# Optimization experiments

Hardware: AMD Instinct MI355X
Metric: run time of the kernel (lower is better)

## Reference

```python
import jax, jax.numpy as jnp
import numpy as np

EPS = 1e-5

def setup_inputs() -> dict:
    key = jax.random.key(0)
    ks = jax.random.split(key, 4)
    B, C, H, W = 32, 256, 32, 32
    x = jax.random.normal(ks[0], (B, C, H, W), dtype=jnp.float32)
    gamma = jnp.ones((C,), dtype=jnp.float32)
    beta = jnp.zeros((C,), dtype=jnp.float32)
    # torch nn.Linear init scale ~ 1/sqrt(fan_in)
    W_kqv = jax.random.normal(ks[1], (3 * C, C), dtype=jnp.float32) / np.sqrt(C)
    b_kqv = jnp.zeros((3 * C,), dtype=jnp.float32)
    W_proj = jax.random.normal(ks[2], (C, C), dtype=jnp.float32) / np.sqrt(C)
    b_proj = jnp.zeros((C,), dtype=jnp.float32)
    return {"x": x, "gamma": gamma, "beta": beta, "W_kqv": W_kqv,
            "b_kqv": b_kqv, "W_proj": W_proj, "b_proj": b_proj}

def reference(x, gamma, beta, W_kqv, b_kqv, W_proj, b_proj):
    B, C, H, W = x.shape
    scale = jnp.sqrt(jnp.asarray(C, dtype=x.dtype))
    # BatchNorm2d (training-mode batch statistics, biased variance, eps=1e-5)
    mean = jnp.mean(x, axis=(0, 2, 3), keepdims=True)
    var = jnp.var(x, axis=(0, 2, 3), keepdims=True)
    t = (x - mean) * jax.lax.rsqrt(var + EPS)
    t = t * gamma[None, :, None, None] + beta[None, :, None, None]
    # [B, C, H, W] -> [B, N, C] with N = H*W
    t = t.reshape(B, C, H * W).transpose(0, 2, 1)
    kqv = t @ W_kqv.T + b_kqv           # [B, N, 3C]
    q, k, v = jnp.split(kqv, 3, axis=-1)  # each [B, N, C]
    s = jnp.einsum('bnc,bmc->bnm', q, k) / scale  # [B, N, N]
    attn = jax.nn.softmax(s, axis=-1)
    o = jnp.einsum('bnm,bmc->bnc', attn, v)        # [B, N, C]
    o = o @ W_proj.T + b_proj
    o = o.transpose(0, 2, 1).reshape(B, C, H, W)
    return o + x
```

## Files before the change

kernel.cpp:

```cpp
#include <hip/hip_runtime.h>

typedef unsigned short u16;
typedef __attribute__((ext_vector_type(8))) short bf16x8;
typedef __attribute__((ext_vector_type(4))) float f32x4;

__device__ __forceinline__ float bf2f(u16 u) {
  union { unsigned u; float f; } c; c.u = ((unsigned)u) << 16; return c.f;
}
__device__ __forceinline__ u16 f2bf(float f) {
  union { float f; unsigned u; } c; c.f = f;
  unsigned u = c.u;
  return (u16)((u + 0x7FFFu + ((u >> 16) & 1u)) >> 16);
}
__device__ __forceinline__ void gld16(const void* g, void* l) {
  __builtin_amdgcn_global_load_lds(
      (__attribute__((address_space(1))) void*)g,
      (__attribute__((address_space(3))) void*)l, 16, 0, 0);
}

#define BB 32
#define CC 256
#define NN 1024

__global__ __launch_bounds__(256) void convert_w_kernel(
    const float* __restrict__ Wk, const float* __restrict__ bk,
    const float* __restrict__ Wp, const float* __restrict__ bp,
    u16* __restrict__ Wkb, u16* __restrict__ bkb,
    u16* __restrict__ Wpb, u16* __restrict__ bpb)
{
  int b = blockIdx.x, t = threadIdx.x;
  const float* src; u16* dst; int idx, n;
  if (b < 768)       { src = Wk; dst = Wkb; idx = b * 256 + t;        n = 196608; }
  else if (b < 771)  { src = bk; dst = bkb; idx = (b - 768) * 256 + t; n = 768;   }
  else if (b < 1027) { src = Wp; dst = Wpb; idx = (b - 771) * 256 + t; n = 65536; }
  else               { src = bp; dst = bpb; idx = t;                  n = 256;    }
  if (idx < n) dst[idx] = f2bf(src[idx]);
}

__global__ __launch_bounds__(256) void bn_stats_kernel(
    const float* __restrict__ x, const float* __restrict__ gamma,
    const float* __restrict__ beta, float* __restrict__ scl, float* __restrict__ sft)
{
  int c = blockIdx.x;
  int tid = threadIdx.x;
  float s = 0.f, q = 0.f;
  for (int g = tid; g < 8192; g += 256) {
    int b = g >> 8;
    int n = (g & 255) * 4;
    float4 v = *reinterpret_cast<const float4*>(x + (((size_t)(b * CC + c)) << 10) + n);
    s += v.x + v.y + v.z + v.w;
    q += v.x * v.x + v.y * v.y + v.z * v.z + v.w * v.w;
  }
  __shared__ float rs[256], rq[256];
  rs[tid] = s; rq[tid] = q;
  __syncthreads();
  for (int off = 128; off > 0; off >>= 1) {
    if (tid < off) { rs[tid] += rs[tid + off]; rq[tid] += rq[tid + off]; }
    __syncthreads();
  }
  if (tid == 0) {
    float mean = rs[0] * (1.f / 32768.f);
    float var  = rq[0] * (1.f / 32768.f) - mean * mean;
    float rstd = rsqrtf(var + 1e-5f);
    float g = gamma[c] * rstd;
    scl[c] = g;
    sft[c] = beta[c] - mean * g;
  }
}

__global__ __launch_bounds__(256) void norm_transpose_kernel(
    const float* __restrict__ x, const float* __restrict__ scl,
    const float* __restrict__ sft, u16* __restrict__ t)
{
  __shared__ float tile[64][65];
  int b = blockIdx.z, n0 = blockIdx.x * 64, c0 = blockIdx.y * 64;
  int tid = threadIdx.x;
  int hi = tid >> 4, lo4 = (tid & 15) * 4;
  #pragma unroll
  for (int r = 0; r < 4; ++r) {
    int cl = r * 16 + hi;
    int c = c0 + cl;
    float4 v = *reinterpret_cast<const float4*>(
        x + (((size_t)(b * CC + c)) << 10) + n0 + lo4);
    float sc = scl[c], sh = sft[c];
    tile[cl][lo4 + 0] = v.x * sc + sh;
    tile[cl][lo4 + 1] = v.y * sc + sh;
    tile[cl][lo4 + 2] = v.z * sc + sh;
    tile[cl][lo4 + 3] = v.w * sc + sh;
  }
  __syncthreads();
  #pragma unroll
  for (int r = 0; r < 4; ++r) {
    int nl = r * 16 + hi;
    ushort4 o;
    o.x = f2bf(tile[lo4 + 0][nl]);
    o.y = f2bf(tile[lo4 + 1][nl]);
    o.z = f2bf(tile[lo4 + 2][nl]);
    o.w = f2bf(tile[lo4 + 3][nl]);
    *reinterpret_cast<ushort4*>(t + ((size_t)(b * NN + n0 + nl)) * CC + c0 + lo4) = o;
  }
}

__global__ __launch_bounds__(256) void gemm_nt_kernel(
    const u16* __restrict__ A, int lda, size_t sA,
    const u16* __restrict__ B, int ldb, size_t sB,
    u16* __restrict__ C, int ldc, size_t sC,
    int K, const u16* __restrict__ bias, float scale, int mode,
    const float* __restrict__ xres, float* __restrict__ outf)
{
  __shared__ u16 As[128 * 32];
  __shared__ u16 Bs[128 * 32];
  int tid = threadIdx.x;
  int m0 = blockIdx.x * 128, n0 = blockIdx.y * 128;
  const u16* Ab = A + (size_t)blockIdx.z * sA;
  const u16* Bb = B + (size_t)blockIdx.z * sB;
  u16* Cb = C + (size_t)blockIdx.z * sC;

  int lane = tid & 63, w = tid >> 6;
  int lq = lane & 15, quad = lane >> 4;
  int wm = (w >> 1) * 64, wn = (w & 1) * 64;
  int ar = lane >> 2, ac = (lane & 3) * 8;
  int rb = w * 32;

  f32x4 zero = {0.f, 0.f, 0.f, 0.f};
  f32x4 acc[4][4];
  #pragma unroll
  for (int i = 0; i < 4; ++i)
    #pragma unroll
    for (int j = 0; j < 4; ++j) acc[i][j] = zero;

  for (int k0 = 0; k0 < K; k0 += 32) {
    __syncthreads();
    gld16(Ab + (size_t)(m0 + rb +      ar) * lda + k0 + ac, &As[(rb     ) * 32]);
    gld16(Ab + (size_t)(m0 + rb + 16 + ar) * lda + k0 + ac, &As[(rb + 16) * 32]);
    gld16(Bb + (size_t)(n0 + rb +      ar) * ldb + k0 + ac, &Bs[(rb     ) * 32]);
    gld16(Bb + (size_t)(n0 + rb + 16 + ar) * ldb + k0 + ac, &Bs[(rb + 16) * 32]);
    __syncthreads();
    bf16x8 af[4], bfr[4];
    #pragma unroll
    for (int i = 0; i < 4; ++i) {
      af[i]  = *reinterpret_cast<const bf16x8*>(&As[(wm + i * 16 + lq) * 32 + quad * 8]);
      bfr[i] = *reinterpret_cast<const bf16x8*>(&Bs[(wn + i * 16 + lq) * 32 + quad * 8]);
    }
    #pragma unroll
    for (int i = 0; i < 4; ++i)
      #pragma unroll
      for (int j = 0; j < 4; ++j)
        acc[i][j] = __builtin_amdgcn_mfma_f32_16x16x32_bf16(af[i], bfr[j], acc[i][j], 0, 0, 0);
  }

  #pragma unroll
  for (int j = 0; j < 4; ++j) {
    int col = n0 + wn + j * 16 + lq;
    float bv = bias ? bf2f(bias[col]) : 0.f;
    #pragma unroll
    for (int i = 0; i < 4; ++i) {
      int rbase = m0 + wm + i * 16 + quad * 4;
      if (mode == 2) {
        int b = rbase >> 10, n = rbase & 1023;
        size_t idx = (((size_t)(b * CC + col)) << 10) + n;
        float4 xv = *reinterpret_cast<const float4*>(xres + idx);
        float4 o;
        o.x = acc[i][j][0] * scale + bv + xv.x;
        o.y = acc[i][j][1] * scale + bv + xv.y;
        o.z = acc[i][j][2] * scale + bv + xv.z;
        o.w = acc[i][j][3] * scale + bv + xv.w;
        *reinterpret_cast<float4*>(outf + idx) = o;
      } else if (mode == 1) {
        int b = rbase >> 10, n = rbase & 1023;
        ushort4 o;
        o.x = f2bf(acc[i][j][0] * scale + bv);
        o.y = f2bf(acc[i][j][1] * scale + bv);
        o.z = f2bf(acc[i][j][2] * scale + bv);
        o.w = f2bf(acc[i][j][3] * scale + bv);
        *reinterpret_cast<ushort4*>(&Cb[(size_t)b * 262144 + (size_t)col * 1024 + n]) = o;
      } else {
        #pragma unroll
        for (int r = 0; r < 4; ++r)
          Cb[(size_t)(rbase + r) * ldc + col] = f2bf(acc[i][j][r] * scale + bv);
      }
    }
  }
}

__global__ __launch_bounds__(256, 1) void attn_kernel(
    const u16* __restrict__ qk,
    const u16* __restrict__ vt,
    u16* __restrict__ o)
{
  __shared__ __align__(16) u16 Ks[2][64 * 256];
  __shared__ __align__(16) u16 Vs[2][256 * 64];
  __shared__ __align__(16) u16 Ps[4][32 * 64];

  int bid = blockIdx.x;
  int b  = (bid & 7) + 8 * ((bid >> 3) & 3);
  int qt = bid >> 5;
  int tid = threadIdx.x, lane = tid & 63, w = tid >> 6;
  int lq = lane & 15, hh = lane >> 4;

  const u16* qb = qk + ((size_t)b << 10) * 512;
  const u16* kb = qb + 256;
  const u16* vb = vt + ((size_t)b << 18);
  int q0 = qt * 128 + w * 32;
  int wslot = tid & 192;

  auto stage = [&](int kt, int bufi) {
    #pragma unroll
    for (int i = 0; i < 8; ++i) {
      int slot = i * 256 + tid;
      int r = slot >> 5, c = slot & 31;
      gld16(kb + (size_t)(kt * 64 + r) * 512 + ((c ^ (r & 7)) << 3),
            &Ks[bufi][(i * 256 + wslot) * 8]);
    }
    #pragma unroll
    for (int i = 0; i < 8; ++i) {
      int slot = i * 256 + tid;
      int n = slot >> 3, c = slot & 7;
      gld16(vb + (size_t)(n << 10) + kt * 64 + ((c ^ (n & 7)) << 3),
            &Vs[bufi][(i * 256 + wslot) * 8]);
    }
  };

  bf16x8 qf[2][8];
  #pragma unroll
  for (int qi = 0; qi < 2; ++qi)
    #pragma unroll
    for (int kk = 0; kk < 8; ++kk)
      qf[qi][kk] = *reinterpret_cast<const bf16x8*>(
          qb + (size_t)(q0 + qi * 16 + lq) * 512 + kk * 32 + hh * 8);

  f32x4 zero = {0.f, 0.f, 0.f, 0.f};
  f32x4 oacc[2][16];
  #pragma unroll
  for (int qi = 0; qi < 2; ++qi)
    #pragma unroll
    for (int nj = 0; nj < 16; ++nj) oacc[qi][nj] = zero;
  float runsum[2][4] = {{0.f, 0.f, 0.f, 0.f}, {0.f, 0.f, 0.f, 0.f}};

  u16* Pw = Ps[w];

  stage(0, 0);
  __syncthreads();

  #pragma unroll 1
  for (int kt = 0; kt < 16; ++kt) {
    int cur = kt & 1;
    if (kt < 15) stage(kt + 1, cur ^ 1);
    const u16* Kc = Ks[cur];
    const u16* Vc = Vs[cur];

    f32x4 sacc[2][4];
    #pragma unroll
    for (int qi = 0; qi < 2; ++qi)
      #pragma unroll
      for (int ni = 0; ni < 4; ++ni) sacc[qi][ni] = zero;
    #pragma unroll
    for (int kk = 0; kk < 8; ++kk) {
      bf16x8 kf[4];
      #pragma unroll
      for (int ni = 0; ni < 4; ++ni) {
        int r = ni * 16 + lq;
        kf[ni] = *reinterpret_cast<const bf16x8*>(
            &Kc[r * 256 + (((kk * 4 + hh) ^ (r & 7)) << 3)]);
      }
      #pragma unroll
      for (int qi = 0; qi < 2; ++qi)
        #pragma unroll
        for (int ni = 0; ni < 4; ++ni)
          sacc[qi][ni] = __builtin_amdgcn_mfma_f32_16x16x32_bf16(
              qf[qi][kk], kf[ni], sacc[qi][ni], 0, 0, 0);
    }

    #pragma unroll
    for (int qi = 0; qi < 2; ++qi)
      #pragma unroll
      for (int ni = 0; ni < 4; ++ni)
        #pragma unroll
        for (int rr = 0; rr < 4; ++rr) {
          float p = __expf(sacc[qi][ni][rr] * 0.0625f);
          u16 pb = f2bf(p);
          runsum[qi][rr] += bf2f(pb);
          int q = qi * 16 + hh * 4 + rr;
          int kcol = ni * 16 + lq;
          Pw[q * 64 + ((((kcol >> 3) ^ (q & 7)) << 3) | (kcol & 7))] = pb;
        }

    #pragma unroll
    for (int kk2 = 0; kk2 < 2; ++kk2) {
      bf16x8 pa[2];
      #pragma unroll
      for (int qi = 0; qi < 2; ++qi) {
        int q = qi * 16 + lq;
        pa[qi] = *reinterpret_cast<const bf16x8*>(
            &Pw[q * 64 + (((kk2 * 4 + hh) ^ (q & 7)) << 3)]);
      }
      #pragma unroll
      for (int nj = 0; nj < 16; ++nj) {
        int n = nj * 16 + lq;
        bf16x8 vf = *reinterpret_cast<const bf16x8*>(
            &Vc[n * 64 + (((kk2 * 4 + hh) ^ (n & 7)) << 3)]);
        #pragma unroll
        for (int qi = 0; qi < 2; ++qi)
          oacc[qi][nj] = __builtin_amdgcn_mfma_f32_16x16x32_bf16(
              pa[qi], vf, oacc[qi][nj], 0, 0, 0);
      }
    }
    __syncthreads();
  }

  #pragma unroll
  for (int qi = 0; qi < 2; ++qi)
    #pragma unroll
    for (int rr = 0; rr < 4; ++rr) {
      float s = runsum[qi][rr];
      s += __shfl_xor(s, 1, 64);
      s += __shfl_xor(s, 2, 64);
      s += __shfl_xor(s, 4, 64);
      s += __shfl_xor(s, 8, 64);
      runsum[qi][rr] = 1.f / s;
    }
  u16* ob = o + (size_t)((b << 10) + q0) * 256;
  #pragma unroll
  for (int qi = 0; qi < 2; ++qi)
    #pragma unroll
    for (int nj = 0; nj < 16; ++nj)
      #pragma unroll
      for (int rr = 0; rr < 4; ++rr)
        ob[(size_t)(qi * 16 + hh * 4 + rr) * 256 + nj * 16 + lq] =
            f2bf(oacc[qi][nj][rr] * runsum[qi][rr]);
}

extern "C" void kernel_launch(void* const* d_in, const int* in_sizes, int n_in,
                              void* d_out, int out_size, void* d_ws, size_t ws_size,
                              hipStream_t stream) {
  const float* x     = (const float*)d_in[0];
  const float* gamma = (const float*)d_in[1];
  const float* beta  = (const float*)d_in[2];
  const float* Wkqv  = (const float*)d_in[3];
  const float* bkqv  = (const float*)d_in[4];
  const float* Wproj = (const float*)d_in[5];
  const float* bproj = (const float*)d_in[6];
  float* out = (float*)d_out;

  char* ws = (char*)d_ws;
  float* scl    = (float*)ws;
  float* sft    = (float*)(ws + 1024);
  u16* Wkb = (u16*)(ws + 4096);
  u16* bkb = Wkb + 196608;
  u16* Wpb = bkb + 768;
  u16* bpb = Wpb + 65536;
  u16* qk   = (u16*)(ws + 1048576);
  u16* vt   = qk + (size_t)32768 * 512;
  u16* o_pv = vt + (size_t)32 * 256 * 1024;
  u16* t = (u16*)d_out;

  convert_w_kernel<<<dim3(1028), dim3(256), 0, stream>>>(
      Wkqv, bkqv, Wproj, bproj, Wkb, bkb, Wpb, bpb);
  bn_stats_kernel<<<dim3(256), dim3(256), 0, stream>>>(x, gamma, beta, scl, sft);
  norm_transpose_kernel<<<dim3(16, 4, 32), dim3(256), 0, stream>>>(x, scl, sft, t);
  gemm_nt_kernel<<<dim3(256, 4, 1), dim3(256), 0, stream>>>(
      t, 256, 0, Wkb, 256, 0, qk, 512, 0, 256, bkb, 1.0f, 0, nullptr, nullptr);
  gemm_nt_kernel<<<dim3(256, 2, 1), dim3(256), 0, stream>>>(
      t, 256, 0, Wkb + 512 * 256, 256, 0, vt, 0, 0, 256, bkb + 512, 1.0f, 1,
      nullptr, nullptr);
  attn_kernel<<<dim3(256), dim3(256), 0, stream>>>(qk, vt, o_pv);
  gemm_nt_kernel<<<dim3(256, 2, 1), dim3(256), 0, stream>>>(
      o_pv, 256, 0, Wpb, 256, 0, nullptr, 0, 0, 256, bpb, 1.0f, 2, x, out);
}
```

Measured before the change: 227.2 us.

## Warp-specialize attention: split QK/softmax and PV waves into a software pipeline

The attention kernel now runs 512 threads, with four waves computing QK^T and exp and four waves computing P·V one tile behind. P is exchanged through a shared 128x64 LDS buffer, and row sums are passed through LDS at the end. The aim is to overlap the softmax/exp work with the PV MFMAs and to give each PV wave a 128x64 output tile, which gives more reuse of V fragments. The cost is two block-wide barriers per tile, LDS traffic for P, and heavier per-wave register use under launch_bounds(512,2) with the same LDS footprint.

```diff
diff --git a/kernel.cpp b/kernel.cpp
--- a/kernel.cpp
+++ b/kernel.cpp
@@ -17,6 +17,12 @@
       (__attribute__((address_space(1))) void*)g,
       (__attribute__((address_space(3))) void*)l, 16, 0, 0);
 }
+
+#define SYNCB() do { \
+  asm volatile("s_waitcnt vmcnt(0) lgkmcnt(0)" ::: "memory"); \
+  __builtin_amdgcn_s_barrier(); \
+  __builtin_amdgcn_sched_barrier(0); \
+} while (0)
 
 #define BB 32
 #define CC 256
@@ -183,151 +189,194 @@
   }
 }
 
-__global__ __launch_bounds__(256, 1) void attn_kernel(
+__global__ __launch_bounds__(512, 2) void attn_kernel(
     const u16* __restrict__ qk,
     const u16* __restrict__ vt,
     u16* __restrict__ o)
 {
   __shared__ __align__(16) u16 Ks[2][64 * 256];
   __shared__ __align__(16) u16 Vs[2][256 * 64];
-  __shared__ __align__(16) u16 Ps[4][32 * 64];
+  __shared__ __align__(16) u16 Ps[128 * 64];
+  float* rs = (float*)Ps;
 
   int bid = blockIdx.x;
   int b  = (bid & 7) + 8 * ((bid >> 3) & 3);
   int qt = bid >> 5;
   int tid = threadIdx.x, lane = tid & 63, w = tid >> 6;
   int lq = lane & 15, hh = lane >> 4;
+  int wr = w & 3;
+  bool isQK = w < 4;
 
   const u16* qb = qk + ((size_t)b << 10) * 512;
   const u16* kb = qb + 256;
   const u16* vb = vt + ((size_t)b << 18);
-  int q0 = qt * 128 + w * 32;
-  int wslot = tid & 192;
-
-  auto stage = [&](int kt, int bufi) {
-    #pragma unroll
-    for (int i = 0; i < 8; ++i) {
-      int slot = i * 256 + tid;
+
+  auto stageK = [&](int kt, int bufi) {
+    #pragma unroll
+    for (int i = 0; i < 4; ++i) {
+      int slot = i * 512 + tid;
       int r = slot >> 5, c = slot & 31;
       gld16(kb + (size_t)(kt * 64 + r) * 512 + ((c ^ (r & 7)) << 3),
-            &Ks[bufi][(i * 256 + wslot) * 8]);
-    }
-    #pragma unroll
-    for (int i = 0; i < 8; ++i) {
-      int slot = i * 256 + tid;
+            &Ks[bufi][(i * 512 + (tid & 448)) * 8]);
+    }
+  };
+  auto stageV = [&](int kt, int bufi) {
+    #pragma unroll
+    for (int i = 0; i < 4; ++i) {
+      int slot = i * 512 + tid;
       int n = slot >> 3, c = slot & 7;
       gld16(vb + (size_t)(n << 10) + kt * 64 + ((c ^ (n & 7)) << 3),
-            &Vs[bufi][(i * 256 + wslot) * 8]);
+            &Vs[bufi][(i * 512 + (tid & 448)) * 8]);
     }
   };
 
-  bf16x8 qf[2][8];
-  #pragma unroll
-  for (int qi = 0; qi < 2; ++qi)
-    #pragma unroll
-    for (int kk = 0; kk < 8; ++kk)
-      qf[qi][kk] = *reinterpret_cast<const bf16x8*>(
-          qb + (size_t)(q0 + qi * 16 + lq) * 512 + kk * 32 + hh * 8);
-
   f32x4 zero = {0.f, 0.f, 0.f, 0.f};
-  f32x4 oacc[2][16];
-  #pragma unroll
-  for (int qi = 0; qi < 2; ++qi)
-    #pragma unroll
-    for (int nj = 0; nj < 16; ++nj) oacc[qi][nj] = zero;
-  float runsum[2][4] = {{0.f, 0.f, 0.f, 0.f}, {0.f, 0.f, 0.f, 0.f}};
-
-  u16* Pw = Ps[w];
-
-  stage(0, 0);
-  __syncthreads();
-
-  #pragma unroll 1
-  for (int kt = 0; kt < 16; ++kt) {
-    int cur = kt & 1;
-    if (kt < 15) stage(kt + 1, cur ^ 1);
-    const u16* Kc = Ks[cur];
-    const u16* Vc = Vs[cur];
-
-    f32x4 sacc[2][4];
+
+  stageK(0, 0);
+  SYNCB();
+
+  if (isQK) {
+    int q0 = qt * 128 + wr * 32;
+    bf16x8 qf[2][8];
     #pragma unroll
     for (int qi = 0; qi < 2; ++qi)
       #pragma unroll
-      for (int ni = 0; ni < 4; ++ni) sacc[qi][ni] = zero;
-    #pragma unroll
-    for (int kk = 0; kk < 8; ++kk) {
-      bf16x8 kf[4];
-      #pragma unroll
-      for (int ni = 0; ni < 4; ++ni) {
-        int r = ni * 16 + lq;
-        kf[ni] = *reinterpret_cast<const bf16x8*>(
-            &Kc[r * 256 + (((kk * 4 + hh) ^ (r & 7)) << 3)]);
+      for (int kk = 0; kk < 8; ++kk)
+        qf[qi][kk] = *reinterpret_cast<const bf16x8*>(
+            qb + (size_t)(q0 + qi * 16 + lq) * 512 + kk * 32 + hh * 8);
+    float runsum[2][4] = {{0.f, 0.f, 0.f, 0.f}, {0.f, 0.f, 0.f, 0.f}};
+
+    #pragma unroll 1
+    for (int p = 0; p <= 16; ++p) {
+      if (p <= 15) stageV(p, p & 1);
+      if (p <= 14) stageK(p + 1, (p + 1) & 1);
+      u16 pbv[2][4][4];
+      if (p <= 15) {
+        const u16* Kc = Ks[p & 1];
+        f32x4 sacc[2][4];
+        #pragma unroll
+        for (int qi = 0; qi < 2; ++qi)
+          #pragma unroll
+          for (int ni = 0; ni < 4; ++ni) sacc[qi][ni] = zero;
+        #pragma unroll
+        for (int kk = 0; kk < 8; ++kk) {
+          bf16x8 kf[4];
+          #pragma unroll
+          for (int ni = 0; ni < 4; ++ni) {
+            int r = ni * 16 + lq;
+            kf[ni] = *reinterpret_cast<const bf16x8*>(
+                &Kc[r * 256 + (((kk * 4 + hh) ^ (r & 7)) << 3)]);
+          }
+          __builtin_amdgcn_s_setprio(1);
+          #pragma unroll
+          for (int qi = 0; qi < 2; ++qi)
+            #pragma unroll
+            for (int ni = 0; ni < 4; ++ni)
+              sacc[qi][ni] = __builtin_amdgcn_mfma_f32_16x16x32_bf16(
+                  qf[qi][kk], kf[ni], sacc[qi][ni], 0, 0, 0);
+          __builtin_amdgcn_s_setprio(0);
+        }
+        #pragma unroll
+        for (int qi = 0; qi < 2; ++qi)
+          #pragma unroll
+          for (int ni = 0; ni < 4; ++ni)
+            #pragma unroll
+            for (int rr = 0; rr < 4; ++rr) {
+              float pexp = __expf(sacc[qi][ni][rr] * 0.0625f);
+              u16 pb = f2bf(pexp);
+              runsum[qi][rr] += bf2f(pb);
+              pbv[qi][ni][rr] = pb;
+            }
       }
-      #pragma unroll
-      for (int qi = 0; qi < 2; ++qi)
-        #pragma unroll
-        for (int ni = 0; ni < 4; ++ni)
-          sacc[qi][ni] = __builtin_amdgcn_mfma_f32_16x16x32_bf16(
-              qf[qi][kk], kf[ni], sacc[qi][ni], 0, 0, 0);
+      SYNCB();
+      if (p <= 15) {
+        #pragma unroll
+        for (int qi = 0; qi < 2; ++qi)
+          #pragma unroll
+          for (int ni = 0; ni < 4; ++ni)
+            #pragma unroll
+            for (int rr = 0; rr < 4; ++rr) {
+              int q = wr * 32 + qi * 16 + hh * 4 + rr;
+              int kcol = ni * 16 + lq;
+              Ps[q * 64 + ((((kcol >> 3) ^ (q & 7)) << 3) | (kcol & 7))] =
+                  pbv[qi][ni][rr];
+            }
+      }
+      SYNCB();
     }
 
     #pragma unroll
     for (int qi = 0; qi < 2; ++qi)
       #pragma unroll
-      for (int ni = 0; ni < 4; ++ni)
-        #pragma unroll
-        for (int rr = 0; rr < 4; ++rr) {
-          float p = __expf(sacc[qi][ni][rr] * 0.0625f);
-          u16 pb = f2bf(p);
-          runsum[qi][rr] += bf2f(pb);
-          int q = qi * 16 + hh * 4 + rr;
-          int kcol = ni * 16 + lq;
-          Pw[q * 64 + ((((kcol >> 3) ^ (q & 7)) << 3) | (kcol & 7))] = pb;
+      for (int rr = 0; rr < 4; ++rr) {
+        float s = runsum[qi][rr];
+        s += __shfl_xor(s, 1, 64);
+        s += __shfl_xor(s, 2, 64);
+        s += __shfl_xor(s, 4, 64);
+        s += __shfl_xor(s, 8, 64);
+        if (lq == 0) rs[wr * 32 + qi * 16 + hh * 4 + rr] = 1.f / s;
+      }
+    SYNCB();
+  } else {
+    f32x4 oacc[8][4];
+    #pragma unroll
+    for (int qi = 0; qi < 8; ++qi)
+      #pragma unroll
+      for (int nj = 0; nj < 4; ++nj) oacc[qi][nj] = zero;
+
+    #pragma unroll 1
+    for (int p = 0; p <= 16; ++p) {
+      if (p <= 15) stageV(p, p & 1);
+      if (p <= 14) stageK(p + 1, (p + 1) & 1);
+      if (p >= 1) {
+        const u16* Vc = Vs[(p - 1) & 1];
+        #pragma unroll
+        for (int kk2 = 0; kk2 < 2; ++kk2) {
+          bf16x8 pa[8];
+          #pragma unroll
+          for (int qi = 0; qi < 8; ++qi) {
+            int r = qi * 16 + lq;
+            pa[qi] = *reinterpret_cast<const bf16x8*>(
+                &Ps[r * 64 + (((kk2 * 4 + hh) ^ (r & 7)) << 3)]);
+          }
+          bf16x8 vf[4];
+          #pragma unroll
+          for (int nj = 0; nj < 4; ++nj) {
+            int n = wr * 64 + nj * 16 + lq;
+            vf[nj] = *reinterpret_cast<const bf16x8*>(
+                &Vc[n * 64 + (((kk2 * 4 + hh) ^ (n & 7)) << 3)]);
+          }
+          __builtin_amdgcn_s_setprio(1);
+          #pragma unroll
+          for (int qi = 0; qi < 8; ++qi)
+            #pragma unroll
+            for (int nj = 0; nj < 4; ++nj)
+              oacc[qi][nj] = __builtin_amdgcn_mfma_f32_16x16x32_bf16(
+                  pa[qi], vf[nj], oacc[qi][nj], 0, 0, 0);
+          __builtin_amdgcn_s_setprio(0);
         }
-
-    #pragma unroll
-    for (int kk2 = 0; kk2 < 2; ++kk2) {
-      bf16x8 pa[2];
-      #pragma unroll
-      for (int qi = 0; qi < 2; ++qi) {
-        int q = qi * 16 + lq;
-        pa[qi] = *reinterpret_cast<const bf16x8*>(
-            &Pw[q * 64 + (((kk2 * 4 + hh) ^ (q & 7)) << 3)]);
       }
-      #pragma unroll
-      for (int nj = 0; nj < 16; ++nj) {
-        int n = nj * 16 + lq;
-        bf16x8 vf = *reinterpret_cast<const bf16x8*>(
-            &Vc[n * 64 + (((kk2 * 4 + hh) ^ (n & 7)) << 3)]);
-        #pragma unroll
-        for (int qi = 0; qi < 2; ++qi)
-          oacc[qi][nj] = __builtin_amdgcn_mfma_f32_16x16x32_bf16(
-              pa[qi], vf, oacc[qi][nj], 0, 0, 0);
-      }
-    }
-    __syncthreads();
-  }
-
-  #pragma unroll
-  for (int qi = 0; qi < 2; ++qi)
-    #pragma unroll
-    for (int rr = 0; rr < 4; ++rr) {
-      float s = runsum[qi][rr];
-      s += __shfl_xor(s, 1, 64);
-      s += __shfl_xor(s, 2, 64);
-      s += __shfl_xor(s, 4, 64);
-      s += __shfl_xor(s, 8, 64);
-      runsum[qi][rr] = 1.f / s;
-    }
-  u16* ob = o + (size_t)((b << 10) + q0) * 256;
-  #pragma unroll
-  for (int qi = 0; qi < 2; ++qi)
-    #pragma unroll
-    for (int nj = 0; nj < 16; ++nj)
+      SYNCB();
+      SYNCB();
+    }
+
+    SYNCB();
+    float rinv[8][4];
+    #pragma unroll
+    for (int qi = 0; qi < 8; ++qi)
       #pragma unroll
       for (int rr = 0; rr < 4; ++rr)
-        ob[(size_t)(qi * 16 + hh * 4 + rr) * 256 + nj * 16 + lq] =
-            f2bf(oacc[qi][nj][rr] * runsum[qi][rr]);
+        rinv[qi][rr] = rs[qi * 16 + hh * 4 + rr];
+    u16* ob = o + ((size_t)(b << 10) + qt * 128) * 256;
+    #pragma unroll
+    for (int qi = 0; qi < 8; ++qi)
+      #pragma unroll
+      for (int nj = 0; nj < 4; ++nj)
+        #pragma unroll
+        for (int rr = 0; rr < 4; ++rr)
+          ob[(size_t)(qi * 16 + hh * 4 + rr) * 256 + wr * 64 + nj * 16 + lq] =
+              f2bf(oacc[qi][nj][rr] * rinv[qi][rr]);
+  }
 }
 
 extern "C" void kernel_launch(void* const* d_in, const int* in_sizes, int n_in,
@@ -363,7 +412,7 @@
   gemm_nt_kernel<<<dim3(256, 2, 1), dim3(256), 0, stream>>>(
       t, 256, 0, Wkb + 512 * 256, 256, 0, vt, 0, 0, 256, bkb + 512, 1.0f, 1,
       nullptr, nullptr);
-  attn_kernel<<<dim3(256), dim3(256), 0, stream>>>(qk, vt, o_pv);
+  attn_kernel<<<dim3(256), dim3(512), 0, stream>>>(qk, vt, o_pv);
   gemm_nt_kernel<<<dim3(256, 2, 1), dim3(256), 0, stream>>>(
       o_pv, 256, 0, Wpb, 256, 0, nullptr, 0, 0, 256, bpb, 1.0f, 2, x, out);
 }
```

Result: faster. 211.9 us (-6.7%).
